# Kernel tuning notes

Hardware: AMD Instinct MI355X
Metric: run time of the kernel (lower is better)

## Reference

```python
import jax, jax.numpy as jnp
import numpy as np

EPS = float(np.finfo(np.float32).eps)
QMIN, QMAX = -128, 127


def setup_inputs() -> dict:
    key = jax.random.key(0)
    k_x, k_w, k_ws, k_b = jax.random.split(key, 4)
    M, K, N = 32768, 1024, 1024
    x = jax.random.normal(k_x, (M, K), dtype=jnp.float32)
    # per-channel symmetrically quantized, transposed weight: [K, N], values in [-128, 127]
    w_int8_t = jax.random.randint(k_w, (K, N), QMIN, QMAX + 1, dtype=jnp.int32).astype(jnp.int8)
    # per-out-channel scales (positive, float; torch uses float64, we use float32)
    w_scales = (jax.random.uniform(k_ws, (N,), dtype=jnp.float32) * 0.02 + 1e-4)
    # preprocessed column sums: w_int8_t.sum(dim=0)
    w_int8_t_sums = w_int8_t.astype(jnp.int32).sum(axis=0)
    bias = jax.random.normal(k_b, (N,), dtype=jnp.float32)
    return {
        "x": x,
        "w_int8_t": w_int8_t,
        "w_scales": w_scales,
        "w_int8_t_sums": w_int8_t_sums,
        "bias": bias,
    }


def reference(x, w_int8_t, w_scales, w_int8_t_sums, bias):
    # ---- dynamically_quantize_per_tensor (affine, int8) ----
    min_neg = jnp.minimum(jnp.min(x), jnp.float32(0.0))
    max_pos = jnp.maximum(jnp.max(x), jnp.float32(0.0))
    x_scale = jnp.maximum((max_pos - min_neg) / jnp.float32(QMAX - QMIN), EPS)
    x_zp = jnp.clip(QMIN - jnp.round(min_neg / x_scale), QMIN, QMAX)  # scalar
    x_q = jnp.clip(jnp.round(x / x_scale) + x_zp, QMIN, QMAX).astype(jnp.int8)

    # ---- int8 matmul with int32 accumulation (safe_int_mm equivalent) ----
    xw_i32 = jnp.matmul(
        x_q.astype(jnp.int32), w_int8_t.astype(jnp.int32)
    )  # [M, N] int32

    # ---- dequant with zero-point correction (quant_int8_matmul) ----
    mm_unscaled = xw_i32.astype(jnp.float32) - x_zp * w_int8_t_sums.astype(jnp.float32)
    y = x_scale * w_scales * mm_unscaled  # broadcast w_scales over N

    # ---- bias add (quant_int8_dynamic_linear) ----
    y = y + bias
    return y.astype(jnp.float32)
```

## Files before the change

kernel.cpp:

```cpp
#include <hip/hip_runtime.h>
#include <stdint.h>

#define M_DIM 32768
#define K_DIM 1024
#define N_DIM 1024

typedef int v4i __attribute__((ext_vector_type(4)));

__device__ __forceinline__ void gld_lds16(const void* g, void* lds) {
    __builtin_amdgcn_global_load_lds(
        (const __attribute__((address_space(1))) unsigned int*)g,
        (__attribute__((address_space(3))) unsigned int*)lds, 16, 0, 0);
}

__global__ void k_prep(const float* __restrict__ x,
                       float* __restrict__ pmin, float* __restrict__ pmax,
                       const int* __restrict__ w, int8_t* __restrict__ wt) {
    int t = threadIdx.x;
    if (blockIdx.x < 1024) {
        long gid = (long)blockIdx.x * 256 + t;
        const float4* x4 = (const float4*)x;
        const long n4 = (long)M_DIM * K_DIM / 4;
        float mn = INFINITY, mx = -INFINITY;
#pragma unroll 4
        for (long i = gid; i < n4; i += 1024 * 256) {
            float4 v = x4[i];
            mn = fminf(mn, fminf(fminf(v.x, v.y), fminf(v.z, v.w)));
            mx = fmaxf(mx, fmaxf(fmaxf(v.x, v.y), fmaxf(v.z, v.w)));
        }
        __shared__ float smn[256], smx[256];
        smn[t] = mn; smx[t] = mx;
        __syncthreads();
        for (int s = 128; s > 0; s >>= 1) {
            if (t < s) {
                smn[t] = fminf(smn[t], smn[t + s]);
                smx[t] = fmaxf(smx[t], smx[t + s]);
            }
            __syncthreads();
        }
        if (t == 0) { pmin[blockIdx.x] = smn[0]; pmax[blockIdx.x] = smx[0]; }
    } else {
        __shared__ int8_t tile[32][33];
        int b = blockIdx.x - 1024;
        int bn = (b & 31) * 32;
        int bk = (b >> 5) * 32;
        int tx = t & 31, ty = t >> 5;
#pragma unroll
        for (int i = 0; i < 32; i += 8)
            tile[ty + i][tx] = (int8_t)w[(long)(bk + ty + i) * N_DIM + bn + tx];
        __syncthreads();
#pragma unroll
        for (int i = 0; i < 32; i += 8)
            wt[(long)(bn + ty + i) * K_DIM + bk + tx] = tile[tx][ty + i];
    }
}

__device__ __forceinline__ unsigned q4(float4 v, float s, float zp) {
    int a = (int)fminf(fmaxf(rintf(v.x / s) + zp, -128.0f), 127.0f);
    int b = (int)fminf(fmaxf(rintf(v.y / s) + zp, -128.0f), 127.0f);
    int c = (int)fminf(fmaxf(rintf(v.z / s) + zp, -128.0f), 127.0f);
    int d = (int)fminf(fmaxf(rintf(v.w / s) + zp, -128.0f), 127.0f);
    return (a & 255) | ((b & 255) << 8) | ((c & 255) << 16) | ((d & 255) << 24);
}

__global__ void k_quant(const float* __restrict__ x,
                        const float* __restrict__ pmin,
                        const float* __restrict__ pmax,
                        float* __restrict__ sp,
                        int8_t* __restrict__ xq) {
    int t = threadIdx.x;
    float mn = INFINITY, mx = -INFINITY;
#pragma unroll
    for (int i = 0; i < 4; i++) {
        mn = fminf(mn, pmin[i * 256 + t]);
        mx = fmaxf(mx, pmax[i * 256 + t]);
    }
    __shared__ float smn[256], smx[256];
    smn[t] = mn; smx[t] = mx;
    __syncthreads();
    for (int ss = 128; ss > 0; ss >>= 1) {
        if (t < ss) {
            smn[t] = fminf(smn[t], smn[t + ss]);
            smx[t] = fmaxf(smx[t], smx[t + ss]);
        }
        __syncthreads();
    }
    float min_neg = fminf(smn[0], 0.0f);
    float max_pos = fmaxf(smx[0], 0.0f);
    float s = (max_pos - min_neg) / 255.0f;
    s = fmaxf(s, 1.1920928955078125e-07f);
    float zp = -128.0f - rintf(min_neg / s);
    zp = fminf(fmaxf(zp, -128.0f), 127.0f);
    if (blockIdx.x == 0 && t == 0) { sp[0] = s; sp[1] = zp; }

    const float4* x4 = (const float4*)x;
    unsigned* q4out = (unsigned*)xq;
    long base = (long)blockIdx.x * 1024;
#pragma unroll
    for (int v = 0; v < 4; v++) {
        long i = base + (long)v * 256 + t;
        float4 val = x4[i];
        q4out[i] = q4(val, s, zp);
    }
}

__global__ __launch_bounds__(256, 3) void k_gemm(
    const int8_t* __restrict__ xq, const int8_t* __restrict__ wt,
    const float* __restrict__ sp, const float* __restrict__ w_scales,
    const int* __restrict__ wsums, const float* __restrict__ bias,
    float* __restrict__ out) {
    __shared__ __align__(16) int8_t lds_a[3][128 * 64];
    __shared__ __align__(16) int8_t lds_b[3][128 * 64];

    const int t = threadIdx.x;
    const int orig = blockIdx.x;
    const int swz = (orig & 7) * 256 + (orig >> 3);
    const int m0 = (swz >> 3) * 128;
    const int n0 = (swz & 7) * 128;
    const int w = t >> 6, l = t & 63, quad = l >> 4, r = l & 15;
    const int wave_m = (w & 1) * 64, wave_n = (w >> 1) * 64;

    v4i acc[4][4];
#pragma unroll
    for (int i = 0; i < 4; i++)
#pragma unroll
        for (int j = 0; j < 4; j++) acc[i][j] = (v4i){0, 0, 0, 0};

    const int slot0 = t, slot1 = 256 + t;
    const int row0 = slot0 >> 2, s0 = slot0 & 3;
    const int row1 = slot1 >> 2, s1 = slot1 & 3;
    const int q0 = s0 ^ (row0 & 3) ^ ((row0 >> 2) & 3);
    const int q1 = s1 ^ (row1 & 3) ^ ((row1 >> 2) & 3);
    const int8_t* gA0 = xq + (long)(m0 + row0) * K_DIM + q0 * 16;
    const int8_t* gA1 = xq + (long)(m0 + row1) * K_DIM + q1 * 16;
    const int8_t* gB0 = wt + (long)(n0 + row0) * K_DIM + q0 * 16;
    const int8_t* gB1 = wt + (long)(n0 + row1) * K_DIM + q1 * 16;

#define STAGE(buf, kb)                                        \
    do {                                                      \
        gld_lds16(gA0 + (kb), lds_a[buf] + slot0 * 16);       \
        gld_lds16(gA1 + (kb), lds_a[buf] + slot1 * 16);       \
        gld_lds16(gB0 + (kb), lds_b[buf] + slot0 * 16);       \
        gld_lds16(gB1 + (kb), lds_b[buf] + slot1 * 16);       \
    } while (0)

    int ra[4], rb[4];
#pragma unroll
    for (int i = 0; i < 4; i++) {
        int mrow = wave_m + i * 16 + r;
        int sa = quad ^ (mrow & 3) ^ ((mrow >> 2) & 3);
        ra[i] = mrow * 64 + sa * 16;
        int nrow = wave_n + i * 16 + r;
        int sb = quad ^ (nrow & 3) ^ ((nrow >> 2) & 3);
        rb[i] = nrow * 64 + sb * 16;
    }

    STAGE(0, 0);
    STAGE(1, 64);

#pragma unroll
    for (int kt = 0; kt < 16; ++kt) {
        if (kt < 15)
            asm volatile("s_waitcnt vmcnt(4)" ::: "memory");
        else
            asm volatile("s_waitcnt vmcnt(0)" ::: "memory");
        asm volatile("s_barrier" ::: "memory");

        if (kt <= 13) STAGE((kt + 2) % 3, (kt + 2) * 64);

        v4i af[4], bf[4];
#pragma unroll
        for (int i = 0; i < 4; i++) af[i] = *(const v4i*)(lds_a[kt % 3] + ra[i]);
#pragma unroll
        for (int j = 0; j < 4; j++) bf[j] = *(const v4i*)(lds_b[kt % 3] + rb[j]);

        __builtin_amdgcn_s_setprio(1);
#pragma unroll
        for (int i = 0; i < 4; i++)
#pragma unroll
            for (int j = 0; j < 4; j++)
                acc[i][j] = __builtin_amdgcn_mfma_i32_16x16x64_i8(af[i], bf[j], acc[i][j], 0, 0, 0);
        __builtin_amdgcn_s_setprio(0);
    }
#undef STAGE

    const float scale = sp[0], zp = sp[1];
#pragma unroll
    for (int j = 0; j < 4; j++) {
        int n = n0 + wave_n + j * 16 + r;
        float sj = scale * w_scales[n];
        float cj = zp * (float)wsums[n];
        float bj = bias[n];
#pragma unroll
        for (int i = 0; i < 4; i++) {
            int mbase = m0 + wave_m + i * 16 + quad * 4;
#pragma unroll
            for (int e = 0; e < 4; e++) {
                out[(long)(mbase + e) * N_DIM + n] = sj * ((float)acc[i][j][e] - cj) + bj;
            }
        }
    }
}

extern "C" void kernel_launch(void* const* d_in, const int* in_sizes, int n_in,
                              void* d_out, int out_size, void* d_ws, size_t ws_size,
                              hipStream_t stream) {
    const float* x        = (const float*)d_in[0];
    const int*   w_int8_t = (const int*)d_in[1];
    const float* w_scales = (const float*)d_in[2];
    const int*   w_sums   = (const int*)d_in[3];
    const float* bias     = (const float*)d_in[4];
    float* out = (float*)d_out;

    float* wsf  = (float*)d_ws;
    float* pmin = wsf;
    float* pmax = wsf + 1024;
    float* sp   = wsf + 2048;
    int8_t* wt  = (int8_t*)d_ws + 16384;
    int8_t* xq  = (int8_t*)d_ws + 16384 + (size_t)K_DIM * N_DIM;

    k_prep<<<2048, 256, 0, stream>>>(x, pmin, pmax, w_int8_t, wt);
    k_quant<<<8192, 256, 0, stream>>>(x, pmin, pmax, sp, xq);
    k_gemm<<<2048, 256, 0, stream>>>(xq, wt, sp, w_scales, w_sums, bias, out);
}
```

Before: 303.4 us.

## Pre-tile quantized operands into MFMA fragment layout and load GEMM directly from global

The quantize kernel and the weight transpose now write xq and wt in a fragment-major layout, where each 16-row by 64-k chunk is stored contiguously. The GEMM can then fetch its MFMA operands straight from global memory into registers, with register double-buffering in place of the LDS triple buffer and its barriers. The quantize kernel is regrouped to 2048 blocks that stage through LDS to perform the reordering. The trade-off is losing LDS-level sharing between waves: each wave reads its own A and B rows, so L2/global traffic rises, and there is no longer an explicit async prefetch pipeline.

```diff
diff --git a/kernel.cpp b/kernel.cpp
--- a/kernel.cpp
+++ b/kernel.cpp
@@ -7,11 +7,6 @@
 
 typedef int v4i __attribute__((ext_vector_type(4)));
 
-__device__ __forceinline__ void gld_lds16(const void* g, void* lds) {
-    __builtin_amdgcn_global_load_lds(
-        (const __attribute__((address_space(1))) unsigned int*)g,
-        (__attribute__((address_space(3))) unsigned int*)lds, 16, 0, 0);
-}
 
 __global__ void k_prep(const float* __restrict__ x,
                        float* __restrict__ pmin, float* __restrict__ pmax,
@@ -50,8 +45,13 @@
             tile[ty + i][tx] = (int8_t)w[(long)(bk + ty + i) * N_DIM + bn + tx];
         __syncthreads();
 #pragma unroll
-        for (int i = 0; i < 32; i += 8)
-            wt[(long)(bn + ty + i) * K_DIM + bk + tx] = tile[tx][ty + i];
+        for (int i = 0; i < 32; i += 8) {
+            int n = bn + ty + i;
+            int k = bk + tx;
+            long addr = (long)(n >> 4) * 16384 + (k >> 6) * 1024 +
+                        ((k >> 4) & 3) * 256 + (n & 15) * 16 + (k & 15);
+            wt[addr] = tile[tx][ty + i];
+        }
     }
 }
 
@@ -68,39 +68,50 @@
                         const float* __restrict__ pmax,
                         float* __restrict__ sp,
                         int8_t* __restrict__ xq) {
-    int t = threadIdx.x;
+    __shared__ unsigned lq[16 * 260];
+    __shared__ float red[2][256];
+
+    const int t = threadIdx.x;
+
     float mn = INFINITY, mx = -INFINITY;
 #pragma unroll
     for (int i = 0; i < 4; i++) {
         mn = fminf(mn, pmin[i * 256 + t]);
         mx = fmaxf(mx, pmax[i * 256 + t]);
     }
-    __shared__ float smn[256], smx[256];
-    smn[t] = mn; smx[t] = mx;
+    red[0][t] = mn; red[1][t] = mx;
     __syncthreads();
     for (int ss = 128; ss > 0; ss >>= 1) {
         if (t < ss) {
-            smn[t] = fminf(smn[t], smn[t + ss]);
-            smx[t] = fmaxf(smx[t], smx[t + ss]);
+            red[0][t] = fminf(red[0][t], red[0][t + ss]);
+            red[1][t] = fmaxf(red[1][t], red[1][t + ss]);
         }
         __syncthreads();
     }
-    float min_neg = fminf(smn[0], 0.0f);
-    float max_pos = fmaxf(smx[0], 0.0f);
+    const float min_neg = fminf(red[0][0], 0.0f);
+    const float max_pos = fmaxf(red[1][0], 0.0f);
     float s = (max_pos - min_neg) / 255.0f;
     s = fmaxf(s, 1.1920928955078125e-07f);
     float zp = -128.0f - rintf(min_neg / s);
     zp = fminf(fmaxf(zp, -128.0f), 127.0f);
     if (blockIdx.x == 0 && t == 0) { sp[0] = s; sp[1] = zp; }
 
-    const float4* x4 = (const float4*)x;
-    unsigned* q4out = (unsigned*)xq;
-    long base = (long)blockIdx.x * 1024;
+    const float4* xp = (const float4*)x + (long)blockIdx.x * 4096;
+#pragma unroll
+    for (int v = 0; v < 16; v++) {
+        int i = v * 256 + t;
+        float4 val = xp[i];
+        lq[(i >> 8) * 260 + (i & 255)] = q4(val, s, zp);
+    }
+    __syncthreads();
+
+    uint4* outp = (uint4*)(xq + (long)blockIdx.x * 16384);
 #pragma unroll
     for (int v = 0; v < 4; v++) {
-        long i = base + (long)v * 256 + t;
-        float4 val = x4[i];
-        q4out[i] = q4(val, s, zp);
+        int c = v * 256 + t;
+        int r = c & 15, q = (c >> 4) & 3, kt = c >> 6;
+        const uint4 val = *(const uint4*)&lq[r * 260 + kt * 16 + q * 4];
+        outp[c] = val;
     }
 }
 
@@ -109,16 +120,17 @@
     const float* __restrict__ sp, const float* __restrict__ w_scales,
     const int* __restrict__ wsums, const float* __restrict__ bias,
     float* __restrict__ out) {
-    __shared__ __align__(16) int8_t lds_a[3][128 * 64];
-    __shared__ __align__(16) int8_t lds_b[3][128 * 64];
-
     const int t = threadIdx.x;
     const int orig = blockIdx.x;
     const int swz = (orig & 7) * 256 + (orig >> 3);
     const int m0 = (swz >> 3) * 128;
     const int n0 = (swz & 7) * 128;
     const int w = t >> 6, l = t & 63, quad = l >> 4, r = l & 15;
-    const int wave_m = (w & 1) * 64, wave_n = (w >> 1) * 64;
+    const int m0w = m0 + (w & 1) * 64;
+    const int n0w = n0 + (w >> 1) * 64;
+
+    const int8_t* pa = xq + (long)m0w * 1024 + l * 16;
+    const int8_t* pb = wt + (long)n0w * 1024 + l * 16;
 
     v4i acc[4][4];
 #pragma unroll
@@ -126,74 +138,43 @@
 #pragma unroll
         for (int j = 0; j < 4; j++) acc[i][j] = (v4i){0, 0, 0, 0};
 
-    const int slot0 = t, slot1 = 256 + t;
-    const int row0 = slot0 >> 2, s0 = slot0 & 3;
-    const int row1 = slot1 >> 2, s1 = slot1 & 3;
-    const int q0 = s0 ^ (row0 & 3) ^ ((row0 >> 2) & 3);
-    const int q1 = s1 ^ (row1 & 3) ^ ((row1 >> 2) & 3);
-    const int8_t* gA0 = xq + (long)(m0 + row0) * K_DIM + q0 * 16;
-    const int8_t* gA1 = xq + (long)(m0 + row1) * K_DIM + q1 * 16;
-    const int8_t* gB0 = wt + (long)(n0 + row0) * K_DIM + q0 * 16;
-    const int8_t* gB1 = wt + (long)(n0 + row1) * K_DIM + q1 * 16;
-
-#define STAGE(buf, kb)                                        \
-    do {                                                      \
-        gld_lds16(gA0 + (kb), lds_a[buf] + slot0 * 16);       \
-        gld_lds16(gA1 + (kb), lds_a[buf] + slot1 * 16);       \
-        gld_lds16(gB0 + (kb), lds_b[buf] + slot0 * 16);       \
-        gld_lds16(gB1 + (kb), lds_b[buf] + slot1 * 16);       \
-    } while (0)
-
-    int ra[4], rb[4];
-#pragma unroll
-    for (int i = 0; i < 4; i++) {
-        int mrow = wave_m + i * 16 + r;
-        int sa = quad ^ (mrow & 3) ^ ((mrow >> 2) & 3);
-        ra[i] = mrow * 64 + sa * 16;
-        int nrow = wave_n + i * 16 + r;
-        int sb = quad ^ (nrow & 3) ^ ((nrow >> 2) & 3);
-        rb[i] = nrow * 64 + sb * 16;
-    }
-
-    STAGE(0, 0);
-    STAGE(1, 64);
+    v4i af[2][4], bf[2][4];
+#pragma unroll
+    for (int i = 0; i < 4; i++) af[0][i] = *(const v4i*)(pa + i * 16384);
+#pragma unroll
+    for (int j = 0; j < 4; j++) bf[0][j] = *(const v4i*)(pb + j * 16384);
 
 #pragma unroll
     for (int kt = 0; kt < 16; ++kt) {
-        if (kt < 15)
-            asm volatile("s_waitcnt vmcnt(4)" ::: "memory");
-        else
-            asm volatile("s_waitcnt vmcnt(0)" ::: "memory");
-        asm volatile("s_barrier" ::: "memory");
-
-        if (kt <= 13) STAGE((kt + 2) % 3, (kt + 2) * 64);
-
-        v4i af[4], bf[4];
-#pragma unroll
-        for (int i = 0; i < 4; i++) af[i] = *(const v4i*)(lds_a[kt % 3] + ra[i]);
-#pragma unroll
-        for (int j = 0; j < 4; j++) bf[j] = *(const v4i*)(lds_b[kt % 3] + rb[j]);
-
+        const int cur = kt & 1, nxt = cur ^ 1;
+        if (kt < 15) {
+#pragma unroll
+            for (int i = 0; i < 4; i++)
+                af[nxt][i] = *(const v4i*)(pa + i * 16384 + (kt + 1) * 1024);
+#pragma unroll
+            for (int j = 0; j < 4; j++)
+                bf[nxt][j] = *(const v4i*)(pb + j * 16384 + (kt + 1) * 1024);
+        }
         __builtin_amdgcn_s_setprio(1);
 #pragma unroll
         for (int i = 0; i < 4; i++)
 #pragma unroll
             for (int j = 0; j < 4; j++)
-                acc[i][j] = __builtin_amdgcn_mfma_i32_16x16x64_i8(af[i], bf[j], acc[i][j], 0, 0, 0);
+                acc[i][j] = __builtin_amdgcn_mfma_i32_16x16x64_i8(
+                    af[cur][i], bf[cur][j], acc[i][j], 0, 0, 0);
         __builtin_amdgcn_s_setprio(0);
     }
-#undef STAGE
 
     const float scale = sp[0], zp = sp[1];
 #pragma unroll
     for (int j = 0; j < 4; j++) {
-        int n = n0 + wave_n + j * 16 + r;
+        int n = n0w + j * 16 + r;
         float sj = scale * w_scales[n];
         float cj = zp * (float)wsums[n];
         float bj = bias[n];
 #pragma unroll
         for (int i = 0; i < 4; i++) {
-            int mbase = m0 + wave_m + i * 16 + quad * 4;
+            int mbase = m0w + i * 16 + quad * 4;
 #pragma unroll
             for (int e = 0; e < 4; e++) {
                 out[(long)(mbase + e) * N_DIM + n] = sj * ((float)acc[i][j][e] - cj) + bj;
@@ -220,6 +201,6 @@
     int8_t* xq  = (int8_t*)d_ws + 16384 + (size_t)K_DIM * N_DIM;
 
     k_prep<<<2048, 256, 0, stream>>>(x, pmin, pmax, w_int8_t, wt);
-    k_quant<<<8192, 256, 0, stream>>>(x, pmin, pmax, sp, xq);
+    k_quant<<<2048, 256, 0, stream>>>(x, pmin, pmax, sp, xq);
     k_gemm<<<2048, 256, 0, stream>>>(xq, wt, sp, w_scales, w_sums, bias, out);
 }
```

Measured after the change: 305.1 us. Within noise of the previous version (+0.6%).
